# Kernel optimization log

Hardware: AMD Instinct MI355X
Metric: run time of the kernel (lower is better)

Reference implementation:

```python
import jax, jax.numpy as jnp
import numpy as np

HIDDEN = 4096
IN_DIM = 784
OUT_DIM = 10
CF = 4  # compression_factor
BATCH = 8192


def _dequant_weight(tile_i32, alphas, out_dim, in_dim):
    """Reconstruct weight: tile (+1/-1, size numel/CF) repeated CF times,
    each repetition (tile_size chunk) scaled by its own alpha, reshaped to [out,in].
    Since chunk i of the tiled vector is exactly the tile, this is alphas[i]*sign."""
    sign = (2 * tile_i32 - 1).astype(alphas.dtype)            # [tile_size], +/-1
    flat = (alphas[:, None] * sign[None, :]).reshape(-1)      # [numel]
    return flat.reshape(out_dim, in_dim)


def setup_inputs() -> dict:
    key = jax.random.key(0)
    k1, k2, k3, k4, k5 = jax.random.split(key, 5)
    x = jax.random.normal(k1, (BATCH, IN_DIM), dtype=jnp.float32)
    tile1 = jax.random.randint(k2, (HIDDEN * IN_DIM // CF,), 0, 2, dtype=jnp.int32)
    alphas1 = jax.random.uniform(k3, (CF,), dtype=jnp.float32)
    tile2 = jax.random.randint(k4, (OUT_DIM * HIDDEN // CF,), 0, 2, dtype=jnp.int32)
    alphas2 = jax.random.uniform(k5, (CF,), dtype=jnp.float32)
    return {"x": x, "tile1": tile1, "alphas1": alphas1, "tile2": tile2, "alphas2": alphas2}


def reference(x, tile1, alphas1, tile2, alphas2):
    w1 = _dequant_weight(tile1, alphas1, HIDDEN, IN_DIM)   # [4096, 784]
    h = jax.nn.relu(x @ w1.T)                              # [B, 4096]
    # NOTE: original forward redundantly recomputes fc1's dequantized weight
    # here and discards it; that is dead code (no effect on output), omitted.
    w2 = _dequant_weight(tile2, alphas2, OUT_DIM, HIDDEN)  # [10, 4096]
    out = h @ w2.T                                         # [B, 10]
    return out
```

## Files before the change

kernel.cpp:

```cpp
#include <hip/hip_runtime.h>

#define B_    8192
#define K_    784
#define KP    832
#define NKB   13
#define RP    1024
#define HID   4096
#define OD    10
#define TS2   10240

#define NB_XQ 1664
#define NB_SQ 208
#define NB_F  64
#define NB_Z  80

typedef __attribute__((ext_vector_type(8))) short  bf16x8;
typedef __attribute__((ext_vector_type(4))) int    i32x4;
typedef __attribute__((ext_vector_type(4))) float  f32x4;

__device__ __forceinline__ unsigned short f2bf(float f) {
    unsigned u = __builtin_bit_cast(unsigned, f);
    u += 0x7fffu + ((u >> 16) & 1u);
    return (unsigned short)(u >> 16);
}
__device__ __forceinline__ int qz32(float v) {
    v = fminf(fmaxf(v * 32.f, -127.f), 127.f);
    return (int)__builtin_rintf(v);
}

__global__ __launch_bounds__(256) void prep(
    const float* __restrict__ x, const int* __restrict__ t1,
    const int* __restrict__ t2, const float* __restrict__ a1,
    const float* __restrict__ a2,
    signed char* __restrict__ Xq, signed char* __restrict__ Sq,
    unsigned short* __restrict__ Vfrag, float* __restrict__ out)
{
    const int b = blockIdx.x;
    if (b < NB_XQ) {
        const int id  = b * 256 + threadIdx.x;
        const int row = id / 52;
        const int rem = id - row * 52;
        const int kb  = rem >> 2;
        const int s   = rem & 3;
        const int xi  = (row >> 1) & 3;
        const int k0  = kb * 64 + ((s ^ xi) << 4);
        i32x4 w = {0, 0, 0, 0};
        if (k0 < K_) {
            const float* xp = x + (size_t)row * K_ + k0;
            #pragma unroll
            for (int g = 0; g < 4; ++g) {
                f32x4 a = *(const f32x4*)(xp + g * 4);
                const int q0 = qz32(a.x), q1 = qz32(a.y);
                const int q2 = qz32(a.z), q3 = qz32(a.w);
                w[g] = (q0 & 255) | ((q1 & 255) << 8) |
                       ((q2 & 255) << 16) | ((q3 & 255) << 24);
            }
        }
        *(i32x4*)(Xq + (size_t)row * KP + kb * 64 + s * 16) = w;
    } else if (b < NB_XQ + NB_SQ) {
        const int id  = (b - NB_XQ) * 256 + threadIdx.x;
        const int row = id / 52;
        const int rem = id - row * 52;
        const int kb  = rem >> 2;
        const int s   = rem & 3;
        const int xi  = (row >> 1) & 3;
        const int k0  = kb * 64 + ((s ^ xi) << 4);
        i32x4 w = {0, 0, 0, 0};
        if (k0 < K_) {
            const int* tp = t1 + (size_t)row * K_ + k0;
            #pragma unroll
            for (int g = 0; g < 4; ++g) {
                int wg = 0;
                #pragma unroll
                for (int j = 0; j < 4; ++j)
                    wg |= (tp[g * 4 + j] ? 0x01 : 0xFF) << (8 * j);
                w[g] = wg;
            }
        }
        *(i32x4*)(Sq + (size_t)row * KP + kb * 64 + s * 16) = w;
    } else if (b < NB_XQ + NB_SQ + NB_F) {
        const int id = (b - NB_XQ - NB_SQ) * 256 + threadIdx.x;
        const int o = id >> 10;
        const int r = id & 1023;
        float v = 0.f;
        if (o < OD) {
            #pragma unroll
            for (int c = 0; c < 4; ++c) {
                const int idx = o * HID + c * RP + r;
                const int ch  = idx / TS2;
                const float w2v = a2[ch] * (float)(2 * t2[idx - ch * TS2] - 1);
                v = fmaf(a1[c], w2v, v);
            }
        }
        Vfrag[(r >> 5) * 512 + (o + 16 * ((r >> 3) & 3)) * 8 + (r & 7)] = f2bf(v);
    } else {
        const int id = (b - NB_XQ - NB_SQ - NB_F) * 256 + threadIdx.x;
        ((f32x4*)out)[id] = (f32x4){0.f, 0.f, 0.f, 0.f};
    }
}

__global__ __launch_bounds__(256, 3) void gemm1(const signed char* __restrict__ Xq,
                                                const signed char* __restrict__ Sq,
                                                const unsigned short* __restrict__ Vfrag,
                                                float* __restrict__ out) {
    __shared__ unsigned char SH[32768];

    const int tid  = threadIdx.x;
    const int lane = tid & 63;
    const int wid  = tid >> 6;

    const int swz = (blockIdx.x & 7) * 64 + (blockIdx.x >> 3);
    const int bm  = (swz >> 3) * 128;
    const int bn  = (swz & 7) * 128;

    const int wr = (wid >> 1) * 64;
    const int wc = (wid & 1) * 64;

    const int srow = lane >> 2;
    const int sslt = (lane & 3) << 4;

    const int kg = lane >> 4;
    const int xr = ((lane & 15) >> 1) & 3;
    const int fsl = (kg ^ xr) << 4;
    const int frow = lane & 15;

    i32x4 acc[4][4] = {};

    for (int kb = 0; kb < NKB; ++kb) {
        #pragma unroll
        for (int i = 0; i < 2; ++i) {
            const int base = wid * 2048 + i * 1024;
            const int row  = (base >> 6) + srow;
            const signed char* ga = Xq + (size_t)(bm + row) * KP + kb * 64 + sslt;
            const signed char* gb = Sq + (size_t)(bn + row) * KP + kb * 64 + sslt;
            __builtin_amdgcn_global_load_lds(
                (const __attribute__((address_space(1))) void*)ga,
                (__attribute__((address_space(3))) void*)(&SH[base + lane * 16]),
                16, 0, 0);
            __builtin_amdgcn_global_load_lds(
                (const __attribute__((address_space(1))) void*)gb,
                (__attribute__((address_space(3))) void*)(&SH[8192 + base + lane * 16]),
                16, 0, 0);
        }
        __syncthreads();

        i32x4 af[4], bfr[4];
        #pragma unroll
        for (int mi = 0; mi < 4; ++mi)
            af[mi] = *(const i32x4*)&SH[(wr + mi * 16 + frow) * 64 + fsl];
        #pragma unroll
        for (int ni = 0; ni < 4; ++ni)
            bfr[ni] = *(const i32x4*)&SH[8192 + (wc + ni * 16 + frow) * 64 + fsl];
        #pragma unroll
        for (int mi = 0; mi < 4; ++mi)
            #pragma unroll
            for (int ni = 0; ni < 4; ++ni)
                acc[mi][ni] = __builtin_amdgcn_mfma_i32_16x16x64_i8(
                    af[mi], bfr[ni], acc[mi][ni], 0, 0, 0);

        __syncthreads();
    }

    unsigned short* Hlds = (unsigned short*)SH;
    #pragma unroll
    for (int mi = 0; mi < 4; ++mi) {
        #pragma unroll
        for (int ni = 0; ni < 4; ++ni) {
            const int col = wc + ni * 16 + (lane & 15);
            #pragma unroll
            for (int r = 0; r < 4; ++r) {
                const int row = wr + mi * 16 + (lane >> 4) * 4 + r;
                const float hv = (float)acc[mi][ni][r] * 0.03125f;
                Hlds[row * 128 + ((((col >> 3) ^ (row & 7)) << 3) | (col & 7))]
                    = f2bf(fmaxf(hv, 0.f));
            }
        }
    }
    __syncthreads();

    const int kb0 = bn >> 5;
    bf16x8 vb[4];
    #pragma unroll
    for (int kk = 0; kk < 4; ++kk)
        vb[kk] = *(const bf16x8*)&Vfrag[(kb0 + kk) * 512 + lane * 8];

    #pragma unroll
    for (int mf = 0; mf < 2; ++mf) {
        const int mloc = (wid * 2 + mf) * 16;
        const int mrow = mloc + (lane & 15);
        f32x4 pac = {};
        #pragma unroll
        for (int kk = 0; kk < 4; ++kk) {
            const int slot = kk * 4 + (lane >> 4);
            bf16x8 ha = *(const bf16x8*)&Hlds[mrow * 128 + ((slot ^ (mrow & 7)) << 3)];
            pac = __builtin_amdgcn_mfma_f32_16x16x32_bf16(ha, vb[kk], pac, 0, 0, 0);
        }
        const int o = lane & 15;
        if (o < OD) {
            #pragma unroll
            for (int r = 0; r < 4; ++r) {
                const int rowg = bm + mloc + (lane >> 4) * 4 + r;
                atomicAdd(&out[(size_t)rowg * OD + o], pac[r]);
            }
        }
    }
}

#define BM 128
#define BN 128
#define BK 16
__global__ __launch_bounds__(256, 2) void fused_tilednn(
    const float* __restrict__ x, const int* __restrict__ tile1,
    const float* __restrict__ alphas1, const int* __restrict__ tile2,
    const float* __restrict__ alphas2, float* __restrict__ out)
{
    __shared__ float XsF[BK][BM];
    __shared__ float SsF[BK][BN];
    __shared__ float Vl[OD][BN];
    const int t = threadIdx.x, tx = t & 15, ty = t >> 4;
    const int bm = blockIdx.x * BM, bn = blockIdx.y * BN;
    for (int e = t; e < OD * BN; e += 256) {
        const int o = e / BN, rl = e - o * BN, rr = bn + rl;
        float v = 0.f;
        #pragma unroll
        for (int c = 0; c < 4; ++c) {
            const int idx = o * HID + c * RP + rr;
            const int ch = idx / TS2;
            v = fmaf(alphas1[c], alphas2[ch] * (float)(2 * tile2[idx - ch * TS2] - 1), v);
        }
        Vl[o][rl] = v;
    }
    float acc[8][8];
    #pragma unroll
    for (int i = 0; i < 8; ++i)
        #pragma unroll
        for (int j = 0; j < 8; ++j) acc[i][j] = 0.f;
    const int lr = t >> 1, lk = (t & 1) << 3;
    const float* xrow = x + (size_t)(bm + lr) * K_;
    const int* srow = tile1 + (size_t)(bn + lr) * K_;
    for (int k0 = 0; k0 < K_; k0 += BK) {
        __syncthreads();
        const float4 xa = *(const float4*)(xrow + k0 + lk);
        const float4 xb = *(const float4*)(xrow + k0 + lk + 4);
        const int4 sa = *(const int4*)(srow + k0 + lk);
        const int4 sb = *(const int4*)(srow + k0 + lk + 4);
        XsF[lk+0][lr]=xa.x; XsF[lk+1][lr]=xa.y; XsF[lk+2][lr]=xa.z; XsF[lk+3][lr]=xa.w;
        XsF[lk+4][lr]=xb.x; XsF[lk+5][lr]=xb.y; XsF[lk+6][lr]=xb.z; XsF[lk+7][lr]=xb.w;
        SsF[lk+0][lr]=(float)(2*sa.x-1); SsF[lk+1][lr]=(float)(2*sa.y-1);
        SsF[lk+2][lr]=(float)(2*sa.z-1); SsF[lk+3][lr]=(float)(2*sa.w-1);
        SsF[lk+4][lr]=(float)(2*sb.x-1); SsF[lk+5][lr]=(float)(2*sb.y-1);
        SsF[lk+6][lr]=(float)(2*sb.z-1); SsF[lk+7][lr]=(float)(2*sb.w-1);
        __syncthreads();
        #pragma unroll
        for (int k = 0; k < BK; ++k) {
            float av[8], bv[8];
            #pragma unroll
            for (int i = 0; i < 8; ++i) av[i] = XsF[k][ty*8+i];
            #pragma unroll
            for (int j = 0; j < 8; ++j) bv[j] = SsF[k][tx*8+j];
            #pragma unroll
            for (int i = 0; i < 8; ++i)
                #pragma unroll
                for (int j = 0; j < 8; ++j) acc[i][j] = fmaf(av[i], bv[j], acc[i][j]);
        }
    }
    #pragma unroll
    for (int i = 0; i < 8; ++i)
        #pragma unroll
        for (int j = 0; j < 8; ++j) acc[i][j] = fmaxf(acc[i][j], 0.f);
    #pragma unroll
    for (int o = 0; o < OD; ++o) {
        float vv[8];
        #pragma unroll
        for (int j = 0; j < 8; ++j) vv[j] = Vl[o][tx*8+j];
        float p[8];
        #pragma unroll
        for (int i = 0; i < 8; ++i) {
            float s = 0.f;
            #pragma unroll
            for (int j = 0; j < 8; ++j) s = fmaf(acc[i][j], vv[j], s);
            p[i] = s;
        }
        #pragma unroll
        for (int m = 8; m >= 1; m >>= 1)
            #pragma unroll
            for (int i = 0; i < 8; ++i) p[i] += __shfl_xor(p[i], m, 16);
        if (tx == 0) {
            #pragma unroll
            for (int i = 0; i < 8; ++i)
                atomicAdd(&out[(size_t)(bm + ty*8 + i) * OD + o], p[i]);
        }
    }
}

extern "C" void kernel_launch(void* const* d_in, const int* in_sizes, int n_in,
                              void* d_out, int out_size, void* d_ws, size_t ws_size,
                              hipStream_t stream) {
    const float* x       = (const float*)d_in[0];
    const int*   tile1   = (const int*)  d_in[1];
    const float* alphas1 = (const float*)d_in[2];
    const int*   tile2   = (const int*)  d_in[3];
    const float* alphas2 = (const float*)d_in[4];
    float*       out     = (float*)d_out;

    const size_t OFF_XQ = 0;
    const size_t OFF_SQ = OFF_XQ + (size_t)B_ * KP;
    const size_t OFF_F  = OFF_SQ + (size_t)RP * KP;
    const size_t NEED   = OFF_F + (size_t)16 * RP * 2;

    if (ws_size < NEED) {
        hipMemsetAsync(out, 0, (size_t)out_size * sizeof(float), stream);
        dim3 grid(B_ / BM, RP / BN);
        fused_tilednn<<<grid, 256, 0, stream>>>(x, tile1, alphas1, tile2, alphas2, out);
        return;
    }

    signed char*    Xq    = (signed char*)((char*)d_ws + OFF_XQ);
    signed char*    Sq    = (signed char*)((char*)d_ws + OFF_SQ);
    unsigned short* Vfrag = (unsigned short*)((char*)d_ws + OFF_F);

    prep<<<NB_XQ + NB_SQ + NB_F + NB_Z, 256, 0, stream>>>(
        x, tile1, tile2, alphas1, alphas2, Xq, Sq, Vfrag, out);
    gemm1<<<512, 256, 0, stream>>>(Xq, Sq, Vfrag, out);
}
```

Before: 28.02 us.

## Double-buffer gemm1 K-loop with 128-wide K tiles and async prefetch

Replaces the single-buffered 13-step K loop (64 bytes per step) with a double-buffered 7-step loop of 128-byte K tiles. The next tile is prefetched into the alternate LDS buffer while the current one is computed, using a vmcnt wait instead of a full sync. K padding grows from 832 to 896 and the prep kernels change to match. LDS doubles to 64KB, occupancy drops from 3 to 2 blocks per CU, and extra zero-padded K work is added.

```diff
diff --git a/kernel.cpp b/kernel.cpp
--- a/kernel.cpp
+++ b/kernel.cpp
@@ -2,15 +2,15 @@
 
 #define B_    8192
 #define K_    784
-#define KP    832
-#define NKB   13
+#define KP    896
+#define NKT   7
 #define RP    1024
 #define HID   4096
 #define OD    10
 #define TS2   10240
 
-#define NB_XQ 1664
-#define NB_SQ 208
+#define NB_XQ 1792
+#define NB_SQ 224
 #define NB_F  64
 #define NB_Z  80
 
@@ -38,8 +38,8 @@
     const int b = blockIdx.x;
     if (b < NB_XQ) {
         const int id  = b * 256 + threadIdx.x;
-        const int row = id / 52;
-        const int rem = id - row * 52;
+        const int row = id / 56;
+        const int rem = id - row * 56;
         const int kb  = rem >> 2;
         const int s   = rem & 3;
         const int xi  = (row >> 1) & 3;
@@ -59,8 +59,8 @@
         *(i32x4*)(Xq + (size_t)row * KP + kb * 64 + s * 16) = w;
     } else if (b < NB_XQ + NB_SQ) {
         const int id  = (b - NB_XQ) * 256 + threadIdx.x;
-        const int row = id / 52;
-        const int rem = id - row * 52;
+        const int row = id / 56;
+        const int rem = id - row * 56;
         const int kb  = rem >> 2;
         const int s   = rem & 3;
         const int xi  = (row >> 1) & 3;
@@ -99,11 +99,11 @@
     }
 }
 
-__global__ __launch_bounds__(256, 3) void gemm1(const signed char* __restrict__ Xq,
+__global__ __launch_bounds__(256, 2) void gemm1(const signed char* __restrict__ Xq,
                                                 const signed char* __restrict__ Sq,
                                                 const unsigned short* __restrict__ Vfrag,
                                                 float* __restrict__ out) {
-    __shared__ unsigned char SH[32768];
+    __shared__ unsigned char SH[65536];
 
     const int tid  = threadIdx.x;
     const int lane = tid & 63;
@@ -119,49 +119,83 @@
     const int srow = lane >> 2;
     const int sslt = (lane & 3) << 4;
 
-    const int kg = lane >> 4;
-    const int xr = ((lane & 15) >> 1) & 3;
-    const int fsl = (kg ^ xr) << 4;
+    const int kg   = lane >> 4;
+    const int xr   = ((lane & 15) >> 1) & 3;
+    const int fsl  = (kg ^ xr) << 4;
     const int frow = lane & 15;
 
     i32x4 acc[4][4] = {};
 
-    for (int kb = 0; kb < NKB; ++kb) {
-        #pragma unroll
-        for (int i = 0; i < 2; ++i) {
-            const int base = wid * 2048 + i * 1024;
-            const int row  = (base >> 6) + srow;
-            const signed char* ga = Xq + (size_t)(bm + row) * KP + kb * 64 + sslt;
-            const signed char* gb = Sq + (size_t)(bn + row) * KP + kb * 64 + sslt;
-            __builtin_amdgcn_global_load_lds(
-                (const __attribute__((address_space(1))) void*)ga,
-                (__attribute__((address_space(3))) void*)(&SH[base + lane * 16]),
-                16, 0, 0);
-            __builtin_amdgcn_global_load_lds(
-                (const __attribute__((address_space(1))) void*)gb,
-                (__attribute__((address_space(3))) void*)(&SH[8192 + base + lane * 16]),
-                16, 0, 0);
-        }
-        __syncthreads();
-
-        i32x4 af[4], bfr[4];
-        #pragma unroll
-        for (int mi = 0; mi < 4; ++mi)
-            af[mi] = *(const i32x4*)&SH[(wr + mi * 16 + frow) * 64 + fsl];
-        #pragma unroll
-        for (int ni = 0; ni < 4; ++ni)
-            bfr[ni] = *(const i32x4*)&SH[8192 + (wc + ni * 16 + frow) * 64 + fsl];
-        #pragma unroll
-        for (int mi = 0; mi < 4; ++mi)
-            #pragma unroll
-            for (int ni = 0; ni < 4; ++ni)
-                acc[mi][ni] = __builtin_amdgcn_mfma_i32_16x16x64_i8(
-                    af[mi], bfr[ni], acc[mi][ni], 0, 0, 0);
-
-        __syncthreads();
-    }
+#define STAGE(T, BUF)                                                           \
+    do {                                                                        \
+        _Pragma("unroll")                                                       \
+        for (int i = 0; i < 2; ++i) {                                           \
+            const int base = wid * 2048 + i * 1024;                             \
+            const int row  = wid * 32 + i * 16 + srow;                          \
+            const signed char* ga = Xq + (size_t)(bm + row) * KP + (T) * 128 + sslt; \
+            const signed char* gb = Sq + (size_t)(bn + row) * KP + (T) * 128 + sslt; \
+            __builtin_amdgcn_global_load_lds(                                   \
+                (const __attribute__((address_space(1))) void*)ga,              \
+                (__attribute__((address_space(3))) void*)                       \
+                    (&SH[(BUF) * 32768 + base + lane * 16]), 16, 0, 0);         \
+            __builtin_amdgcn_global_load_lds(                                   \
+                (const __attribute__((address_space(1))) void*)(ga + 64),       \
+                (__attribute__((address_space(3))) void*)                       \
+                    (&SH[(BUF) * 32768 + 8192 + base + lane * 16]), 16, 0, 0);  \
+            __builtin_amdgcn_global_load_lds(                                   \
+                (const __attribute__((address_space(1))) void*)gb,              \
+                (__attribute__((address_space(3))) void*)                       \
+                    (&SH[(BUF) * 32768 + 16384 + base + lane * 16]), 16, 0, 0); \
+            __builtin_amdgcn_global_load_lds(                                   \
+                (const __attribute__((address_space(1))) void*)(gb + 64),       \
+                (__attribute__((address_space(3))) void*)                       \
+                    (&SH[(BUF) * 32768 + 24576 + base + lane * 16]), 16, 0, 0); \
+        }                                                                       \
+    } while (0)
+
+#define COMPUTE(BUF)                                                            \
+    do {                                                                        \
+        _Pragma("unroll")                                                       \
+        for (int half = 0; half < 2; ++half) {                                  \
+            i32x4 af[4], bfr[4];                                                \
+            _Pragma("unroll")                                                   \
+            for (int mi = 0; mi < 4; ++mi)                                      \
+                af[mi] = *(const i32x4*)&SH[(BUF) * 32768 + half * 8192         \
+                                            + (wr + mi * 16 + frow) * 64 + fsl];\
+            _Pragma("unroll")                                                   \
+            for (int ni = 0; ni < 4; ++ni)                                      \
+                bfr[ni] = *(const i32x4*)&SH[(BUF) * 32768 + 16384 + half * 8192\
+                                             + (wc + ni * 16 + frow) * 64 + fsl];\
+            _Pragma("unroll")                                                   \
+            for (int mi = 0; mi < 4; ++mi)                                      \
+                _Pragma("unroll")                                               \
+                for (int ni = 0; ni < 4; ++ni)                                  \
+                    acc[mi][ni] = __builtin_amdgcn_mfma_i32_16x16x64_i8(        \
+                        af[mi], bfr[ni], acc[mi][ni], 0, 0, 0);                 \
+        }                                                                       \
+    } while (0)
+
+    STAGE(0, 0);
+
+    for (int t = 0; t < NKT; ++t) {
+        const int cur = t & 1;
+        if (t + 1 < NKT) {
+            STAGE(t + 1, cur ^ 1);
+            asm volatile("s_waitcnt vmcnt(8)" ::: "memory");
+        } else {
+            asm volatile("s_waitcnt vmcnt(0)" ::: "memory");
+        }
+        __builtin_amdgcn_s_barrier();
+        __builtin_amdgcn_sched_barrier(0);
+        COMPUTE(cur);
+        __builtin_amdgcn_sched_barrier(0);
+        __builtin_amdgcn_s_barrier();
+    }
+#undef STAGE
+#undef COMPUTE
 
     unsigned short* Hlds = (unsigned short*)SH;
+    __syncthreads();
     #pragma unroll
     for (int mi = 0; mi < 4; ++mi) {
         #pragma unroll
```

New measurement: 25.45 us (median of 2 runs). 9.2% less time.

## Prepack X into MFMA fragment order and double-buffer a 128-wide K pipeline

Applied to the files above, without the earlier changes.

The prep kernel now writes quantized X directly in per-lane MFMA fragment order. gemm1 loads the A operand straight from global memory into registers and no longer stages it through LDS. The B operand is double-buffered in LDS with K steps of 128, and explicit vmcnt waits plus raw barriers let the next tile's loads overlap the current MFMAs. This removes half the LDS traffic and one barrier per iteration, but it raises register pressure (launch bounds drop to 2 blocks per SM) and the X workspace grows slightly from padding to 896.

```diff
diff --git a/kernel.cpp b/kernel.cpp
--- a/kernel.cpp
+++ b/kernel.cpp
@@ -2,14 +2,14 @@
 
 #define B_    8192
 #define K_    784
-#define KP    832
-#define NKB   13
+#define KP2   832
+#define NKT   7
 #define RP    1024
 #define HID   4096
 #define OD    10
 #define TS2   10240
 
-#define NB_XQ 1664
+#define NB_XQ 1792
 #define NB_SQ 208
 #define NB_F  64
 #define NB_Z  80
@@ -32,18 +32,20 @@
     const float* __restrict__ x, const int* __restrict__ t1,
     const int* __restrict__ t2, const float* __restrict__ a1,
     const float* __restrict__ a2,
-    signed char* __restrict__ Xq, signed char* __restrict__ Sq,
+    signed char* __restrict__ Xqf, signed char* __restrict__ Sq,
     unsigned short* __restrict__ Vfrag, float* __restrict__ out)
 {
     const int b = blockIdx.x;
     if (b < NB_XQ) {
-        const int id  = b * 256 + threadIdx.x;
-        const int row = id / 52;
-        const int rem = id - row * 52;
-        const int kb  = rem >> 2;
-        const int s   = rem & 3;
-        const int xi  = (row >> 1) & 3;
-        const int k0  = kb * 64 + ((s ^ xi) << 4);
+        const int id   = b * 256 + threadIdx.x;
+        const int lane = id & 63;
+        const int fid  = id >> 6;
+        const int h    = fid & 1;
+        const int q    = fid >> 1;
+        const int t    = q % 7;
+        const int pm   = q / 7;
+        const int row  = (pm >> 3) * 128 + (pm & 7) * 16 + (lane & 15);
+        const int k0   = t * 128 + h * 64 + ((lane >> 4) << 4);
         i32x4 w = {0, 0, 0, 0};
         if (k0 < K_) {
             const float* xp = x + (size_t)row * K_ + k0;
@@ -56,7 +58,7 @@
                        ((q2 & 255) << 16) | ((q3 & 255) << 24);
             }
         }
-        *(i32x4*)(Xq + (size_t)row * KP + kb * 64 + s * 16) = w;
+        *(i32x4*)(Xqf + (size_t)id * 16) = w;
     } else if (b < NB_XQ + NB_SQ) {
         const int id  = (b - NB_XQ) * 256 + threadIdx.x;
         const int row = id / 52;
@@ -77,7 +79,7 @@
                 w[g] = wg;
             }
         }
-        *(i32x4*)(Sq + (size_t)row * KP + kb * 64 + s * 16) = w;
+        *(i32x4*)(Sq + (size_t)row * KP2 + kb * 64 + s * 16) = w;
     } else if (b < NB_XQ + NB_SQ + NB_F) {
         const int id = (b - NB_XQ - NB_SQ) * 256 + threadIdx.x;
         const int o = id >> 10;
@@ -99,7 +101,7 @@
     }
 }
 
-__global__ __launch_bounds__(256, 3) void gemm1(const signed char* __restrict__ Xq,
+__global__ __launch_bounds__(256, 2) void gemm1(const signed char* __restrict__ Xqf,
                                                 const signed char* __restrict__ Sq,
                                                 const unsigned short* __restrict__ Vfrag,
                                                 float* __restrict__ out) {
@@ -119,49 +121,93 @@
     const int srow = lane >> 2;
     const int sslt = (lane & 3) << 4;
 
-    const int kg = lane >> 4;
-    const int xr = ((lane & 15) >> 1) & 3;
-    const int fsl = (kg ^ xr) << 4;
+    const int kg   = lane >> 4;
+    const int xr   = ((lane & 15) >> 1) & 3;
+    const int fsl  = (kg ^ xr) << 4;
     const int frow = lane & 15;
 
+    const int wrMi = (wid >> 1) * 4;
+    const signed char* ap = Xqf + (size_t)(bm >> 7) * 114688
+                                + (size_t)wrMi * 14336 + lane * 16;
+
     i32x4 acc[4][4] = {};
-
-    for (int kb = 0; kb < NKB; ++kb) {
-        #pragma unroll
-        for (int i = 0; i < 2; ++i) {
-            const int base = wid * 2048 + i * 1024;
-            const int row  = (base >> 6) + srow;
-            const signed char* ga = Xq + (size_t)(bm + row) * KP + kb * 64 + sslt;
-            const signed char* gb = Sq + (size_t)(bn + row) * KP + kb * 64 + sslt;
-            __builtin_amdgcn_global_load_lds(
-                (const __attribute__((address_space(1))) void*)ga,
-                (__attribute__((address_space(3))) void*)(&SH[base + lane * 16]),
-                16, 0, 0);
-            __builtin_amdgcn_global_load_lds(
-                (const __attribute__((address_space(1))) void*)gb,
-                (__attribute__((address_space(3))) void*)(&SH[8192 + base + lane * 16]),
-                16, 0, 0);
-        }
-        __syncthreads();
-
-        i32x4 af[4], bfr[4];
-        #pragma unroll
-        for (int mi = 0; mi < 4; ++mi)
-            af[mi] = *(const i32x4*)&SH[(wr + mi * 16 + frow) * 64 + fsl];
-        #pragma unroll
-        for (int ni = 0; ni < 4; ++ni)
-            bfr[ni] = *(const i32x4*)&SH[8192 + (wc + ni * 16 + frow) * 64 + fsl];
-        #pragma unroll
-        for (int mi = 0; mi < 4; ++mi)
-            #pragma unroll
-            for (int ni = 0; ni < 4; ++ni)
-                acc[mi][ni] = __builtin_amdgcn_mfma_i32_16x16x64_i8(
-                    af[mi], bfr[ni], acc[mi][ni], 0, 0, 0);
-
-        __syncthreads();
-    }
+    i32x4 aA[2][8];
+
+#define STAGE_B(T, NXT, NH)                                                     \
+    do {                                                                        \
+        _Pragma("unroll")                                                       \
+        for (int i = 0; i < 2; ++i) {                                           \
+            const int row = wid * 32 + i * 16 + srow;                           \
+            const signed char* gb = Sq + (size_t)(bn + row) * KP2 + (T) * 128 + sslt; \
+            __builtin_amdgcn_global_load_lds(                                   \
+                (const __attribute__((address_space(1))) void*)gb,              \
+                (__attribute__((address_space(3))) void*)                       \
+                    (&SH[(NXT) * 16384 + wid * 2048 + i * 1024 + lane * 16]),   \
+                16, 0, 0);                                                      \
+            if ((NH) == 2)                                                      \
+                __builtin_amdgcn_global_load_lds(                               \
+                    (const __attribute__((address_space(1))) void*)(gb + 64),   \
+                    (__attribute__((address_space(3))) void*)                   \
+                        (&SH[(NXT) * 16384 + 8192 + wid * 2048 + i * 1024 + lane * 16]), \
+                    16, 0, 0);                                                  \
+        }                                                                       \
+    } while (0)
+
+#define LOAD_A(T, NXT, NH)                                                      \
+    do {                                                                        \
+        _Pragma("unroll")                                                       \
+        for (int h = 0; h < (NH); ++h)                                          \
+            _Pragma("unroll")                                                   \
+            for (int mi = 0; mi < 4; ++mi)                                      \
+                aA[NXT][h * 4 + mi] =                                           \
+                    *(const i32x4*)(ap + mi * 14336 + (T) * 2048 + h * 1024);   \
+    } while (0)
+
+    STAGE_B(0, 0, 2);
+    LOAD_A(0, 0, 2);
+
+    #pragma unroll
+    for (int t = 0; t < NKT; ++t) {
+        const int cur = t & 1;
+        if (t < 5) {
+            STAGE_B(t + 1, cur ^ 1, 2);
+            LOAD_A(t + 1, cur ^ 1, 2);
+            asm volatile("s_waitcnt vmcnt(12)" ::: "memory");
+        } else if (t == 5) {
+            STAGE_B(6, cur ^ 1, 1);
+            LOAD_A(6, cur ^ 1, 1);
+            asm volatile("s_waitcnt vmcnt(6)" ::: "memory");
+        } else {
+            asm volatile("s_waitcnt vmcnt(0)" ::: "memory");
+        }
+        __builtin_amdgcn_s_barrier();
+        __builtin_amdgcn_sched_barrier(0);
+
+        const int halves = (t == NKT - 1) ? 1 : 2;
+        #pragma unroll
+        for (int h = 0; h < 2; ++h) {
+            if (h < halves) {
+                i32x4 bfr[4];
+                #pragma unroll
+                for (int ni = 0; ni < 4; ++ni)
+                    bfr[ni] = *(const i32x4*)&SH[cur * 16384 + h * 8192
+                                                 + (wc + ni * 16 + frow) * 64 + fsl];
+                #pragma unroll
+                for (int mi = 0; mi < 4; ++mi)
+                    #pragma unroll
+                    for (int ni = 0; ni < 4; ++ni)
+                        acc[mi][ni] = __builtin_amdgcn_mfma_i32_16x16x64_i8(
+                            aA[cur][h * 4 + mi], bfr[ni], acc[mi][ni], 0, 0, 0);
+            }
+        }
+        __builtin_amdgcn_sched_barrier(0);
+        __builtin_amdgcn_s_barrier();
+    }
+#undef STAGE_B
+#undef LOAD_A
 
     unsigned short* Hlds = (unsigned short*)SH;
+    __syncthreads();
     #pragma unroll
     for (int mi = 0; mi < 4; ++mi) {
         #pragma unroll
@@ -304,8 +350,8 @@
     float*       out     = (float*)d_out;
 
     const size_t OFF_XQ = 0;
-    const size_t OFF_SQ = OFF_XQ + (size_t)B_ * KP;
-    const size_t OFF_F  = OFF_SQ + (size_t)RP * KP;
+    const size_t OFF_SQ = OFF_XQ + (size_t)7168 * 1024;
+    const size_t OFF_F  = OFF_SQ + (size_t)RP * KP2;
     const size_t NEED   = OFF_F + (size_t)16 * RP * 2;
 
     if (ws_size < NEED) {
@@ -315,11 +361,11 @@
         return;
     }
 
-    signed char*    Xq    = (signed char*)((char*)d_ws + OFF_XQ);
+    signed char*    Xqf   = (signed char*)((char*)d_ws + OFF_XQ);
     signed char*    Sq    = (signed char*)((char*)d_ws + OFF_SQ);
     unsigned short* Vfrag = (unsigned short*)((char*)d_ws + OFF_F);
 
     prep<<<NB_XQ + NB_SQ + NB_F + NB_Z, 256, 0, stream>>>(
-        x, tile1, tile2, alphas1, alphas2, Xq, Sq, Vfrag, out);
-    gemm1<<<512, 256, 0, stream>>>(Xq, Sq, Vfrag, out);
-}
+        x, tile1, tile2, alphas1, alphas2, Xqf, Sq, Vfrag, out);
+    gemm1<<<512, 256, 0, stream>>>(Xqf, Sq, Vfrag, out);
+}
```

Result: faster. 26.13 us (-6.7%).
